# Kernel tuning notes

Hardware: AMD Instinct MI355X
Metric: run time of the kernel (lower is better)

## Reference

```python
import jax, jax.numpy as jnp
import numpy as np

D_MODEL = 1024
HEADS = 16
D_K = D_MODEL // HEADS


def setup_inputs() -> dict:
    key = jax.random.key(0)
    ks = jax.random.split(key, 11)
    bs, seq = 2, 2048
    scale = 1.0 / np.sqrt(D_MODEL)
    inp = {
        "query": jax.random.normal(ks[0], (bs, seq, D_MODEL), jnp.float32),
        "key": jax.random.normal(ks[1], (bs, seq, D_MODEL), jnp.float32),
        "value": jax.random.normal(ks[2], (bs, seq, D_MODEL), jnp.float32),
        # nn.Linear weights: y = x @ W.T + b, W shape [out, in]
        "Wq": jax.random.normal(ks[3], (D_MODEL, D_MODEL), jnp.float32) * scale,
        "bq": jnp.zeros((D_MODEL,), jnp.float32),
        "Wk": jax.random.normal(ks[4], (D_MODEL, D_MODEL), jnp.float32) * scale,
        "bk": jnp.zeros((D_MODEL,), jnp.float32),
        "Wv": jax.random.normal(ks[5], (D_MODEL, D_MODEL), jnp.float32) * scale,
        "bv": jnp.zeros((D_MODEL,), jnp.float32),
        "Wo": jax.random.normal(ks[6], (D_MODEL, D_MODEL), jnp.float32) * scale,
        "bo": jnp.zeros((D_MODEL,), jnp.float32),
    }
    return inp


def _split_heads(x, bs):
    # [b, s, d_model] -> [b, h, s, d_k]
    return x.reshape(bs, -1, HEADS, D_K).transpose(0, 2, 1, 3)


def reference(query, key, value, Wq, bq, Wk, bk, Wv, bv, Wo, bo):
    bs = query.shape[0]
    q = _split_heads(query @ Wq.T + bq, bs)
    k = _split_heads(key @ Wk.T + bk, bs)
    v = _split_heads(value @ Wv.T + bv, bs)
    # scaled dot-product attention (dropout is identity at eval)
    logits = jnp.einsum("bhqd,bhkd->bhqk", q, k) / np.sqrt(D_K).astype(np.float32)
    probs = jax.nn.softmax(logits, axis=-1)
    scores = jnp.einsum("bhqk,bhkd->bhqd", probs, v)  # [b, h, s, d_k]
    concat = scores.transpose(0, 2, 1, 3).reshape(bs, -1, D_MODEL)
    output = concat @ Wo.T + bo
    return (output, scores)
```

## Files before the change

kernel.cpp:

```cpp
#include <hip/hip_runtime.h>
#include <stdint.h>
#include <math.h>

typedef __bf16 bf16;
typedef __bf16 bf16x4 __attribute__((ext_vector_type(4)));
typedef __bf16 bf16x8 __attribute__((ext_vector_type(8)));
typedef float floatx4 __attribute__((ext_vector_type(4)));

#define CEXP 0.1803368801111204f

__global__ __launch_bounds__(256) void wcvt_kernel(
    const float* __restrict__ Wq, const float* __restrict__ Wk,
    const float* __restrict__ Wv, const float* __restrict__ Wo,
    bf16* __restrict__ dst)
{
  const float* src = (blockIdx.y == 0) ? Wq : (blockIdx.y == 1) ? Wk
                   : (blockIdx.y == 2) ? Wv : Wo;
  bf16* d = dst + (size_t)blockIdx.y * 1048576;
  const int i = (blockIdx.x * 256 + threadIdx.x) * 4;
  const floatx4 v = *(const floatx4*)(src + i);
  bf16x4 o;
#pragma unroll
  for (int j = 0; j < 4; ++j) o[j] = (bf16)v[j];
  *(bf16x4*)(d + i) = o;
}

__device__ __forceinline__ void gemm_body(
    const float* __restrict__ A, const bf16* __restrict__ Ab,
    const bf16* __restrict__ Wb, const float* __restrict__ bias,
    void* __restrict__ Cout, const int mode, const float oscale)
{
  __shared__ __align__(16) bf16 As[128 * 72];
  __shared__ __align__(16) bf16 Bs[128 * 72];
  const int tid  = threadIdx.x;
  const int wave = tid >> 6;
  const int lane = tid & 63;
  const int mlane = lane & 15;
  const int quad  = lane >> 4;
  const int m0 = blockIdx.x * 128;
  const int n0 = blockIdx.y * 128;
  const int wm = (wave >> 1) * 64;
  const int wn = (wave & 1) * 64;
  const int arow = tid >> 4, ac4 = (tid & 15) * 4;
  const int wrow = tid >> 3, wc8 = (tid & 7) * 8;

  floatx4 a_pf[8];
  bf16x8  ab_pf[4];
  bf16x8  w_pf[4];

  auto load_a = [&](int k0) {
    if (mode == 1) {
#pragma unroll
      for (int c = 0; c < 4; ++c) {
        const int token = m0 + c * 32 + wrow;
        const int b = token >> 11, s = token & 2047;
        const int h = k0 >> 6;
        ab_pf[c] = *(const bf16x8*)(Ab + (((size_t)(b * 16 + h) * 2048 + s) << 6) + wc8);
      }
    } else {
#pragma unroll
      for (int rr = 0; rr < 8; ++rr)
        a_pf[rr] = *(const floatx4*)(A + (size_t)(m0 + rr * 16 + arow) * 1024 + k0 + ac4);
    }
  };
  auto load_w = [&](int k0) {
#pragma unroll
    for (int c = 0; c < 4; ++c)
      w_pf[c] = *(const bf16x8*)(Wb + (size_t)(n0 + c * 32 + wrow) * 1024 + k0 + wc8);
  };

  load_a(0);
  load_w(0);

  floatx4 acc[4][4] = {};

  for (int k0 = 0; k0 < 1024; k0 += 64) {
    if (mode == 1) {
#pragma unroll
      for (int c = 0; c < 4; ++c)
        *(bf16x8*)&As[(c * 32 + wrow) * 72 + wc8] = ab_pf[c];
    } else {
#pragma unroll
      for (int rr = 0; rr < 8; ++rr) {
        bf16x4 ac;
#pragma unroll
        for (int j = 0; j < 4; ++j) ac[j] = (bf16)a_pf[rr][j];
        *(bf16x4*)&As[(rr * 16 + arow) * 72 + ac4] = ac;
      }
    }
#pragma unroll
    for (int c = 0; c < 4; ++c)
      *(bf16x8*)&Bs[(c * 32 + wrow) * 72 + wc8] = w_pf[c];
    __syncthreads();

    if (k0 + 64 < 1024) { load_a(k0 + 64); load_w(k0 + 64); }

#pragma unroll
    for (int kk = 0; kk < 64; kk += 32) {
      bf16x8 af[4], bfr[4];
#pragma unroll
      for (int t = 0; t < 4; ++t) {
        af[t]  = *(const bf16x8*)&As[(wm + t * 16 + mlane) * 72 + kk + quad * 8];
        bfr[t] = *(const bf16x8*)&Bs[(wn + t * 16 + mlane) * 72 + kk + quad * 8];
      }
#pragma unroll
      for (int mt = 0; mt < 4; ++mt)
#pragma unroll
        for (int nt = 0; nt < 4; ++nt)
          acc[mt][nt] = __builtin_amdgcn_mfma_f32_16x16x32_bf16(
              af[mt], bfr[nt], acc[mt][nt], 0, 0, 0);
    }
    __syncthreads();
  }

  if (mode == 2) {
    bf16* T = (wave < 2) ? &As[wave * 4608] : &Bs[(wave - 2) * 4608];
#pragma unroll
    for (int nt = 0; nt < 4; ++nt) {
      const float bv = bias[n0 + wn + nt * 16 + mlane];
#pragma unroll
      for (int mt = 0; mt < 4; ++mt) {
        bf16x4 t4;
#pragma unroll
        for (int r = 0; r < 4; ++r)
          t4[r] = (bf16)((acc[mt][nt][r] + bv) * oscale);
        *(bf16x4*)&T[(nt * 16 + mlane) * 72 + mt * 16 + quad * 4] = t4;
      }
    }
    asm volatile("s_waitcnt lgkmcnt(0)" ::: "memory");
    const int token0 = m0 + wm;
    const int bb = token0 >> 11;
    const int srow0 = token0 & 2047;
    const int h = (n0 + wn) >> 6;
    const int dl = lane >> 3;
    const int s8 = (lane & 7) * 8;
    bf16* outp = (bf16*)Cout + ((size_t)(bb * 16 + h) << 17);
#pragma unroll
    for (int p = 0; p < 8; ++p) {
      const int dk = p * 8 + dl;
      const bf16x8 v8 = *(const bf16x8*)&T[dk * 72 + s8];
      *(bf16x8*)&outp[((size_t)dk << 11) + srow0 + s8] = v8;
    }
    return;
  }

#pragma unroll
  for (int nt = 0; nt < 4; ++nt) {
    const int col = n0 + wn + nt * 16 + mlane;
    const float bv = bias[col];
#pragma unroll
    for (int mt = 0; mt < 4; ++mt) {
#pragma unroll
      for (int r = 0; r < 4; ++r) {
        const int row = m0 + wm + mt * 16 + quad * 4 + r;
        const float v = (acc[mt][nt][r] + bv) * oscale;
        if (mode == 0) {
          const int b = row >> 11, s = row & 2047;
          const int h = col >> 6, dk = col & 63;
          ((bf16*)Cout)[(((size_t)(b * 16 + h) * 2048 + s) << 6) + dk] = (bf16)v;
        } else {
          ((float*)Cout)[(size_t)row * 1024 + col] = v;
        }
      }
    }
  }
}

__global__ __launch_bounds__(256) void qkv_kernel(
    const float* __restrict__ q, const float* __restrict__ k, const float* __restrict__ v,
    const bf16* __restrict__ Wb,
    const float* __restrict__ bq, const float* __restrict__ bk, const float* __restrict__ bv,
    bf16* __restrict__ Qw, bf16* __restrict__ Kw, bf16* __restrict__ Vw)
{
  const int z = blockIdx.z;
  const float* A = (z == 0) ? q : (z == 1) ? k : v;
  const bf16* W  = Wb + (size_t)z * 1048576;
  const float* B = (z == 0) ? bq : (z == 1) ? bk : bv;
  if (z == 2)      gemm_body(A, nullptr, W, B, Vw, 2, 1.0f);
  else if (z == 1) gemm_body(A, nullptr, W, B, Kw, 0, 1.0f);
  else             gemm_body(A, nullptr, W, B, Qw, 0, CEXP);
}

__global__ __launch_bounds__(256) void out_kernel(
    const bf16* __restrict__ Sb, const bf16* __restrict__ Wob,
    const float* __restrict__ bo, float* __restrict__ out)
{
  gemm_body(nullptr, Sb, Wob, bo, out, 1, 1.0f);
}

__global__ __launch_bounds__(256) void attn_kernel(
    const bf16* __restrict__ Qw, const bf16* __restrict__ Kw,
    const bf16* __restrict__ Vtg, float* __restrict__ scores,
    bf16* __restrict__ Sb)
{
  __shared__ __align__(16) bf16 Ks[64 * 72];
  __shared__ __align__(16) bf16 Vt[64 * 72];
  __shared__ __align__(16) bf16 Ps[4][16 * 72];

  const int tid  = threadIdx.x;
  const int wave = tid >> 6;
  const int lane = tid & 63;
  const int mlane = lane & 15;
  const int quad  = lane >> 4;

  const int g = blockIdx.x + (blockIdx.y << 5);
  const int slot = g >> 3;
  const int bh = ((g & 7) << 2) + (slot >> 5);
  const int q0 = (slot & 31) << 6;
  const size_t base = (size_t)bh << 17;

  const int srow = tid >> 3, sc8 = (tid & 7) * 8;

  bf16x8 qf[2];
#pragma unroll
  for (int c = 0; c < 2; ++c)
    qf[c] = *(const bf16x8*)
        &Qw[base + (size_t)(q0 + wave * 16 + mlane) * 64 + c * 32 + quad * 8];

  bf16x8 ones;
#pragma unroll
  for (int j = 0; j < 8; ++j) ones[j] = (bf16)1.0f;

  floatx4 o[4] = {};
  floatx4 osum = {};

  bf16x8 kpf[2], vpf[2];
  auto load_kv = [&](int kt) {
#pragma unroll
    for (int rr = 0; rr < 2; ++rr) {
      const int row = rr * 32 + srow;
      kpf[rr] = *(const bf16x8*)&Kw[base + (size_t)(kt + row) * 64 + sc8];
      vpf[rr] = *(const bf16x8*)&Vtg[base + (size_t)row * 2048 + kt + sc8];
    }
  };
  load_kv(0);

  for (int kt = 0; kt < 2048; kt += 64) {
    __syncthreads();
#pragma unroll
    for (int rr = 0; rr < 2; ++rr) {
      const int row = rr * 32 + srow;
      *(bf16x8*)&Ks[row * 72 + sc8] = kpf[rr];
      *(bf16x8*)&Vt[row * 72 + sc8] = vpf[rr];
    }
    __syncthreads();
    if (kt + 64 < 2048) load_kv(kt + 64);

#pragma unroll
    for (int nt = 0; nt < 4; ++nt) {
      bf16x8 a0 = *(const bf16x8*)&Ks[(nt * 16 + mlane) * 72 + quad * 8];
      bf16x8 a1 = *(const bf16x8*)&Ks[(nt * 16 + mlane) * 72 + 32 + quad * 8];
      floatx4 s0 = {};
      __builtin_amdgcn_s_setprio(1);
      s0 = __builtin_amdgcn_mfma_f32_16x16x32_bf16(a0, qf[0], s0, 0, 0, 0);
      s0 = __builtin_amdgcn_mfma_f32_16x16x32_bf16(a1, qf[1], s0, 0, 0, 0);
      __builtin_amdgcn_s_setprio(0);
      bf16x4 pk;
#pragma unroll
      for (int r = 0; r < 4; ++r) pk[r] = (bf16)exp2f(s0[r]);
      *(bf16x4*)&Ps[wave][mlane * 72 + nt * 16 + quad * 4] = pk;
    }

    asm volatile("s_waitcnt lgkmcnt(0)" ::: "memory");

    bf16x8 pa0 = *(const bf16x8*)&Ps[wave][mlane * 72 + quad * 8];
    bf16x8 pa1 = *(const bf16x8*)&Ps[wave][mlane * 72 + 32 + quad * 8];
    __builtin_amdgcn_s_setprio(1);
    osum = __builtin_amdgcn_mfma_f32_16x16x32_bf16(pa0, ones, osum, 0, 0, 0);
    osum = __builtin_amdgcn_mfma_f32_16x16x32_bf16(pa1, ones, osum, 0, 0, 0);
#pragma unroll
    for (int nt = 0; nt < 4; ++nt) {
      bf16x8 vb0 = *(const bf16x8*)&Vt[(nt * 16 + mlane) * 72 + quad * 8];
      bf16x8 vb1 = *(const bf16x8*)&Vt[(nt * 16 + mlane) * 72 + 32 + quad * 8];
      o[nt] = __builtin_amdgcn_mfma_f32_16x16x32_bf16(pa0, vb0, o[nt], 0, 0, 0);
      o[nt] = __builtin_amdgcn_mfma_f32_16x16x32_bf16(pa1, vb1, o[nt], 0, 0, 0);
    }
    __builtin_amdgcn_s_setprio(0);
  }

#pragma unroll
  for (int r = 0; r < 4; ++r) {
    const float inv = 1.0f / osum[r];
    const int row = q0 + wave * 16 + quad * 4 + r;
#pragma unroll
    for (int nt = 0; nt < 4; ++nt) {
      const float val = o[nt][r] * inv;
      const size_t idx = base + (size_t)row * 64 + nt * 16 + mlane;
      scores[idx] = val;
      Sb[idx] = (bf16)val;
    }
  }
}

extern "C" void kernel_launch(void* const* d_in, const int* in_sizes, int n_in,
                              void* d_out, int out_size, void* d_ws, size_t ws_size,
                              hipStream_t stream) {
  const float* query = (const float*)d_in[0];
  const float* key   = (const float*)d_in[1];
  const float* value = (const float*)d_in[2];
  const float* Wq = (const float*)d_in[3];
  const float* bq = (const float*)d_in[4];
  const float* Wk = (const float*)d_in[5];
  const float* bk = (const float*)d_in[6];
  const float* Wv = (const float*)d_in[7];
  const float* bv = (const float*)d_in[8];
  const float* Wo = (const float*)d_in[9];
  const float* bo = (const float*)d_in[10];

  float* out    = (float*)d_out;
  float* scores = out + (size_t)4194304;

  bf16* Wb  = (bf16*)d_ws;
  bf16* Qws = Wb + (size_t)4194304;
  bf16* Kws = Qws + (size_t)4194304;
  bf16* Vws = Kws + (size_t)4194304;
  bf16* Sb  = Vws + (size_t)4194304;

  wcvt_kernel<<<dim3(1024, 4), 256, 0, stream>>>(Wq, Wk, Wv, Wo, Wb);
  qkv_kernel<<<dim3(32, 8, 3), 256, 0, stream>>>(query, key, value, Wb,
                                                 bq, bk, bv, Qws, Kws, Vws);
  attn_kernel<<<dim3(32, 32), 256, 0, stream>>>(Qws, Kws, Vws, scores, Sb);
  out_kernel<<<dim3(32, 8), 256, 0, stream>>>(Sb, Wb + (size_t)3145728, bo, out);
}
```

Before: 242.9 us.

## Restructure attention kernel with 32x32 MFMA, 128-query tiles and split-K wave reduction

Each attention block now handles 128 queries instead of 64. The four waves split the work as two query halves by two key halves, and the partial outputs and row sums are reduced through shared memory at the end. The kernel moves from 16x16x32 to 32x32x16 bf16 MFMAs, computes row sums in scalar code instead of with a ones-matrix MFMA, and swaps the padded LDS layout for XOR-swizzled rows. This doubles reuse of each loaded K/V tile and cuts per-tile MFMA overhead. The cost is more registers (launch bounds set to 2), a larger LDS footprint for the reduction buffers, and half as many blocks.

```diff
diff --git a/kernel.cpp b/kernel.cpp
--- a/kernel.cpp
+++ b/kernel.cpp
@@ -6,6 +6,7 @@
 typedef __bf16 bf16x4 __attribute__((ext_vector_type(4)));
 typedef __bf16 bf16x8 __attribute__((ext_vector_type(8)));
 typedef float floatx4 __attribute__((ext_vector_type(4)));
+typedef float floatx16 __attribute__((ext_vector_type(16)));
 
 #define CEXP 0.1803368801111204f
 
@@ -188,49 +189,53 @@
   gemm_body(nullptr, Sb, Wob, bo, out, 1, 1.0f);
 }
 
-__global__ __launch_bounds__(256) void attn_kernel(
+__global__ __launch_bounds__(256, 2) void attn_kernel(
     const bf16* __restrict__ Qw, const bf16* __restrict__ Kw,
     const bf16* __restrict__ Vtg, float* __restrict__ scores,
     bf16* __restrict__ Sb)
 {
-  __shared__ __align__(16) bf16 Ks[64 * 72];
-  __shared__ __align__(16) bf16 Vt[64 * 72];
-  __shared__ __align__(16) bf16 Ps[4][16 * 72];
+  __shared__ __align__(16) char smem[32768];
+  __shared__ __align__(16) float Ored[2][64][64];
+  __shared__ float RSred[2][64][2];
 
   const int tid  = threadIdx.x;
   const int wave = tid >> 6;
   const int lane = tid & 63;
-  const int mlane = lane & 15;
-  const int quad  = lane >> 4;
-
-  const int g = blockIdx.x + (blockIdx.y << 5);
+  const int c    = lane & 31;
+  const int hi   = lane >> 5;
+
+  const int g = blockIdx.x + (blockIdx.y << 4);
   const int slot = g >> 3;
-  const int bh = ((g & 7) << 2) + (slot >> 5);
-  const int q0 = (slot & 31) << 6;
+  const int bh = ((g & 7) << 2) + (slot >> 4);
+  const int q0 = (slot & 15) << 7;
   const size_t base = (size_t)bh << 17;
 
-  const int srow = tid >> 3, sc8 = (tid & 7) * 8;
-
-  bf16x8 qf[2];
-#pragma unroll
-  for (int c = 0; c < 2; ++c)
-    qf[c] = *(const bf16x8*)
-        &Qw[base + (size_t)(q0 + wave * 16 + mlane) * 64 + c * 32 + quad * 8];
-
-  bf16x8 ones;
-#pragma unroll
-  for (int j = 0; j < 8; ++j) ones[j] = (bf16)1.0f;
-
-  floatx4 o[4] = {};
-  floatx4 osum = {};
+  const int qh = (wave & 1) * 64;
+  const int kh = (wave >> 1) * 32;
+
+  const int srow = tid >> 3;
+  const int scb  = (tid & 7) * 16;
+
+  char* Pw = smem + 16384 + wave * 4096;
+
+  bf16x8 qf[2][4];
+#pragma unroll
+  for (int qt = 0; qt < 2; ++qt)
+#pragma unroll
+    for (int m = 0; m < 4; ++m)
+      qf[qt][m] = *(const bf16x8*)
+          &Qw[base + (size_t)(q0 + qh + qt * 32 + c) * 64 + m * 16 + hi * 8];
+
+  floatx16 o[2][2] = {};
+  float rs[2] = {0.f, 0.f};
 
   bf16x8 kpf[2], vpf[2];
   auto load_kv = [&](int kt) {
 #pragma unroll
     for (int rr = 0; rr < 2; ++rr) {
       const int row = rr * 32 + srow;
-      kpf[rr] = *(const bf16x8*)&Kw[base + (size_t)(kt + row) * 64 + sc8];
-      vpf[rr] = *(const bf16x8*)&Vtg[base + (size_t)row * 2048 + kt + sc8];
+      kpf[rr] = *(const bf16x8*)&Kw[base + (size_t)(kt + row) * 64 + (tid & 7) * 8];
+      vpf[rr] = *(const bf16x8*)&Vtg[base + (size_t)row * 2048 + kt + (tid & 7) * 8];
     }
   };
   load_kv(0);
@@ -240,55 +245,122 @@
 #pragma unroll
     for (int rr = 0; rr < 2; ++rr) {
       const int row = rr * 32 + srow;
-      *(bf16x8*)&Ks[row * 72 + sc8] = kpf[rr];
-      *(bf16x8*)&Vt[row * 72 + sc8] = vpf[rr];
+      const int swz = (row & 7) << 4;
+      *(bf16x8*)(smem +        row * 128 + (scb ^ swz)) = kpf[rr];
+      *(bf16x8*)(smem + 8192 + row * 128 + (scb ^ swz)) = vpf[rr];
     }
     __syncthreads();
     if (kt + 64 < 2048) load_kv(kt + 64);
 
-#pragma unroll
-    for (int nt = 0; nt < 4; ++nt) {
-      bf16x8 a0 = *(const bf16x8*)&Ks[(nt * 16 + mlane) * 72 + quad * 8];
-      bf16x8 a1 = *(const bf16x8*)&Ks[(nt * 16 + mlane) * 72 + 32 + quad * 8];
-      floatx4 s0 = {};
+    floatx16 s[2] = {};
+    {
+      const int row = kh + c;
+      const int swz = (row & 7) << 4;
       __builtin_amdgcn_s_setprio(1);
-      s0 = __builtin_amdgcn_mfma_f32_16x16x32_bf16(a0, qf[0], s0, 0, 0, 0);
-      s0 = __builtin_amdgcn_mfma_f32_16x16x32_bf16(a1, qf[1], s0, 0, 0, 0);
+#pragma unroll
+      for (int m = 0; m < 4; ++m) {
+        const bf16x8 a = *(const bf16x8*)(smem + row * 128 + ((m * 32 + hi * 16) ^ swz));
+        s[0] = __builtin_amdgcn_mfma_f32_32x32x16_bf16(a, qf[0][m], s[0], 0, 0, 0);
+        s[1] = __builtin_amdgcn_mfma_f32_32x32x16_bf16(a, qf[1][m], s[1], 0, 0, 0);
+      }
       __builtin_amdgcn_s_setprio(0);
-      bf16x4 pk;
-#pragma unroll
-      for (int r = 0; r < 4; ++r) pk[r] = (bf16)exp2f(s0[r]);
-      *(bf16x4*)&Ps[wave][mlane * 72 + nt * 16 + quad * 4] = pk;
-    }
-
-    asm volatile("s_waitcnt lgkmcnt(0)" ::: "memory");
-
-    bf16x8 pa0 = *(const bf16x8*)&Ps[wave][mlane * 72 + quad * 8];
-    bf16x8 pa1 = *(const bf16x8*)&Ps[wave][mlane * 72 + 32 + quad * 8];
+    }
+
+#pragma unroll
+    for (int qt = 0; qt < 2; ++qt) {
+      char* pr = Pw + (qt * 32 + c) * 64;
+      const int psw = (c & 3) << 4;
+#pragma unroll
+      for (int gg = 0; gg < 4; ++gg) {
+        bf16x4 pk;
+#pragma unroll
+        for (int i = 0; i < 4; ++i) {
+          const float p = exp2f(s[qt][gg * 4 + i]);
+          rs[qt] += p;
+          pk[i] = (bf16)p;
+        }
+        *(bf16x4*)(pr + ((gg * 16 + hi * 8) ^ psw)) = pk;
+      }
+    }
+
     __builtin_amdgcn_s_setprio(1);
-    osum = __builtin_amdgcn_mfma_f32_16x16x32_bf16(pa0, ones, osum, 0, 0, 0);
-    osum = __builtin_amdgcn_mfma_f32_16x16x32_bf16(pa1, ones, osum, 0, 0, 0);
-#pragma unroll
-    for (int nt = 0; nt < 4; ++nt) {
-      bf16x8 vb0 = *(const bf16x8*)&Vt[(nt * 16 + mlane) * 72 + quad * 8];
-      bf16x8 vb1 = *(const bf16x8*)&Vt[(nt * 16 + mlane) * 72 + 32 + quad * 8];
-      o[nt] = __builtin_amdgcn_mfma_f32_16x16x32_bf16(pa0, vb0, o[nt], 0, 0, 0);
-      o[nt] = __builtin_amdgcn_mfma_f32_16x16x32_bf16(pa1, vb1, o[nt], 0, 0, 0);
+#pragma unroll
+    for (int t = 0; t < 2; ++t) {
+      bf16x8 pb[2];
+#pragma unroll
+      for (int qt = 0; qt < 2; ++qt)
+        pb[qt] = *(const bf16x8*)(Pw + (qt * 32 + c) * 64 + ((t * 32 + hi * 16) ^ ((c & 3) << 4)));
+#pragma unroll
+      for (int d = 0; d < 2; ++d) {
+        const int row = d * 32 + c;
+        const bf16x8 va = *(const bf16x8*)
+            (smem + 8192 + row * 128 + ((kh * 2 + t * 32 + hi * 16) ^ ((row & 7) << 4)));
+        o[d][0] = __builtin_amdgcn_mfma_f32_32x32x16_bf16(va, pb[0], o[d][0], 0, 0, 0);
+        o[d][1] = __builtin_amdgcn_mfma_f32_32x32x16_bf16(va, pb[1], o[d][1], 0, 0, 0);
+      }
     }
     __builtin_amdgcn_s_setprio(0);
   }
 
-#pragma unroll
-  for (int r = 0; r < 4; ++r) {
-    const float inv = 1.0f / osum[r];
-    const int row = q0 + wave * 16 + quad * 4 + r;
-#pragma unroll
-    for (int nt = 0; nt < 4; ++nt) {
-      const float val = o[nt][r] * inv;
-      const size_t idx = base + (size_t)row * 64 + nt * 16 + mlane;
-      scores[idx] = val;
-      Sb[idx] = (bf16)val;
-    }
+  rs[0] += __shfl_xor(rs[0], 32, 64);
+  rs[1] += __shfl_xor(rs[1], 32, 64);
+
+  if (wave >= 2) {
+#pragma unroll
+    for (int d = 0; d < 2; ++d)
+#pragma unroll
+      for (int qt = 0; qt < 2; ++qt)
+#pragma unroll
+        for (int gg = 0; gg < 4; ++gg) {
+          floatx4 w4;
+#pragma unroll
+          for (int i = 0; i < 4; ++i) w4[i] = o[d][qt][gg * 4 + i];
+          *(floatx4*)&Ored[wave - 2][lane][(d * 2 + qt) * 16 + gg * 4] = w4;
+        }
+    RSred[wave - 2][lane][0] = rs[0];
+    RSred[wave - 2][lane][1] = rs[1];
+  }
+  __syncthreads();
+  if (wave >= 2) return;
+
+#pragma unroll
+  for (int d = 0; d < 2; ++d)
+#pragma unroll
+    for (int qt = 0; qt < 2; ++qt)
+#pragma unroll
+      for (int gg = 0; gg < 4; ++gg) {
+        const floatx4 r4 = *(const floatx4*)&Ored[wave][lane][(d * 2 + qt) * 16 + gg * 4];
+#pragma unroll
+        for (int i = 0; i < 4; ++i) o[d][qt][gg * 4 + i] += r4[i];
+      }
+  rs[0] += RSred[wave][lane][0];
+  rs[1] += RSred[wave][lane][1];
+
+  const float inv0 = 1.0f / rs[0];
+  const float inv1 = 1.0f / rs[1];
+
+#pragma unroll
+  for (int qt = 0; qt < 2; ++qt) {
+    const float inv = qt ? inv1 : inv0;
+    const int q = q0 + qh + qt * 32 + c;
+    float* sr = scores + base + (size_t)q * 64;
+    bf16*  br = Sb + base + (size_t)q * 64;
+#pragma unroll
+    for (int d = 0; d < 2; ++d)
+#pragma unroll
+      for (int gg = 0; gg < 4; ++gg) {
+        const int dk = d * 32 + gg * 8 + hi * 4;
+        floatx4 v4;
+        bf16x4 b4;
+#pragma unroll
+        for (int i = 0; i < 4; ++i) {
+          const float v = o[d][qt][gg * 4 + i] * inv;
+          v4[i] = v;
+          b4[i] = (bf16)v;
+        }
+        *(floatx4*)(sr + dk) = v4;
+        *(bf16x4*)(br + dk) = b4;
+      }
   }
 }
 
@@ -319,6 +391,6 @@
   wcvt_kernel<<<dim3(1024, 4), 256, 0, stream>>>(Wq, Wk, Wv, Wo, Wb);
   qkv_kernel<<<dim3(32, 8, 3), 256, 0, stream>>>(query, key, value, Wb,
                                                  bq, bk, bv, Qws, Kws, Vws);
-  attn_kernel<<<dim3(32, 32), 256, 0, stream>>>(Qws, Kws, Vws, scores, Sb);
+  attn_kernel<<<dim3(16, 32), 256, 0, stream>>>(Qws, Kws, Vws, scores, Sb);
   out_kernel<<<dim3(32, 8), 256, 0, stream>>>(Sb, Wb + (size_t)3145728, bo, out);
 }
```

After: 245.2 us. About the same (+1.0%).

## Rewrite attention with 32x32 MFMA and register-resident probabilities via permlane swap

Applied to the files above, without the earlier changes.

The attention kernel now uses 32x32x16 bf16 MFMA tiles with 128 queries per block (32 per wave), halving the grid. Softmax probabilities stay in registers: they are packed with v_cvt_pk_bf16_f32 and rearranged with v_permlane32_swap instead of round-tripping through a shared-memory P buffer. The row sum is accumulated in scalar registers instead of an extra MFMA against ones. This cuts LDS traffic and MFMA count per tile, at the cost of higher register pressure and fewer blocks in the grid.

```diff
diff --git a/kernel.cpp b/kernel.cpp
--- a/kernel.cpp
+++ b/kernel.cpp
@@ -6,6 +6,7 @@
 typedef __bf16 bf16x4 __attribute__((ext_vector_type(4)));
 typedef __bf16 bf16x8 __attribute__((ext_vector_type(8)));
 typedef float floatx4 __attribute__((ext_vector_type(4)));
+typedef float floatx16 __attribute__((ext_vector_type(16)));
 
 #define CEXP 0.1803368801111204f
 
@@ -188,108 +189,140 @@
   gemm_body(nullptr, Sb, Wob, bo, out, 1, 1.0f);
 }
 
-__global__ __launch_bounds__(256) void attn_kernel(
+__global__ __launch_bounds__(256, 2) void attn_kernel(
     const bf16* __restrict__ Qw, const bf16* __restrict__ Kw,
     const bf16* __restrict__ Vtg, float* __restrict__ scores,
     bf16* __restrict__ Sb)
 {
-  __shared__ __align__(16) bf16 Ks[64 * 72];
-  __shared__ __align__(16) bf16 Vt[64 * 72];
-  __shared__ __align__(16) bf16 Ps[4][16 * 72];
+  __shared__ __align__(16) char smem[2 * 64 * 136];
+  char* KsB = smem;
+  char* VsB = smem + 64 * 136;
 
   const int tid  = threadIdx.x;
   const int wave = tid >> 6;
   const int lane = tid & 63;
-  const int mlane = lane & 15;
-  const int quad  = lane >> 4;
-
-  const int g = blockIdx.x + (blockIdx.y << 5);
+  const int c    = lane & 31;
+  const int hi   = lane >> 5;
+
+  const int g = blockIdx.x + (blockIdx.y << 4);
   const int slot = g >> 3;
-  const int bh = ((g & 7) << 2) + (slot >> 5);
-  const int q0 = (slot & 31) << 6;
+  const int bh = ((g & 7) << 2) + (slot >> 4);
+  const int q0 = (slot & 15) << 7;
   const size_t base = (size_t)bh << 17;
 
-  const int srow = tid >> 3, sc8 = (tid & 7) * 8;
-
-  bf16x8 qf[2];
-#pragma unroll
-  for (int c = 0; c < 2; ++c)
-    qf[c] = *(const bf16x8*)
-        &Qw[base + (size_t)(q0 + wave * 16 + mlane) * 64 + c * 32 + quad * 8];
-
-  bf16x8 ones;
-#pragma unroll
-  for (int j = 0; j < 8; ++j) ones[j] = (bf16)1.0f;
-
-  floatx4 o[4] = {};
-  floatx4 osum = {};
+  const int srow = tid >> 2;
+  const int sce  = (tid & 3) * 16;
+
+  bf16x8 qf[4];
+#pragma unroll
+  for (int m = 0; m < 4; ++m)
+    qf[m] = *(const bf16x8*)
+        &Qw[base + (size_t)(q0 + wave * 32 + c) * 64 + m * 16 + hi * 8];
+
+  floatx16 o[2] = {};
+  float rs = 0.f;
 
   bf16x8 kpf[2], vpf[2];
   auto load_kv = [&](int kt) {
-#pragma unroll
-    for (int rr = 0; rr < 2; ++rr) {
-      const int row = rr * 32 + srow;
-      kpf[rr] = *(const bf16x8*)&Kw[base + (size_t)(kt + row) * 64 + sc8];
-      vpf[rr] = *(const bf16x8*)&Vtg[base + (size_t)row * 2048 + kt + sc8];
-    }
+    const bf16* kp = &Kw[base + (size_t)(kt + srow) * 64 + sce];
+    kpf[0] = *(const bf16x8*)kp;
+    kpf[1] = *(const bf16x8*)(kp + 8);
+    const bf16* vp = &Vtg[base + (size_t)srow * 2048 + kt + sce];
+    vpf[0] = *(const bf16x8*)vp;
+    vpf[1] = *(const bf16x8*)(vp + 8);
   };
   load_kv(0);
 
   for (int kt = 0; kt < 2048; kt += 64) {
     __syncthreads();
-#pragma unroll
-    for (int rr = 0; rr < 2; ++rr) {
-      const int row = rr * 32 + srow;
-      *(bf16x8*)&Ks[row * 72 + sc8] = kpf[rr];
-      *(bf16x8*)&Vt[row * 72 + sc8] = vpf[rr];
+    {
+      char* kr = KsB + srow * 136 + (tid & 3) * 32;
+      char* vr = VsB + srow * 136 + (tid & 3) * 32;
+      *(bf16x4*)(kr +  0) = ((const bf16x4*)&kpf[0])[0];
+      *(bf16x4*)(kr +  8) = ((const bf16x4*)&kpf[0])[1];
+      *(bf16x4*)(kr + 16) = ((const bf16x4*)&kpf[1])[0];
+      *(bf16x4*)(kr + 24) = ((const bf16x4*)&kpf[1])[1];
+      *(bf16x4*)(vr +  0) = ((const bf16x4*)&vpf[0])[0];
+      *(bf16x4*)(vr +  8) = ((const bf16x4*)&vpf[0])[1];
+      *(bf16x4*)(vr + 16) = ((const bf16x4*)&vpf[1])[0];
+      *(bf16x4*)(vr + 24) = ((const bf16x4*)&vpf[1])[1];
     }
     __syncthreads();
     if (kt + 64 < 2048) load_kv(kt + 64);
 
 #pragma unroll
-    for (int nt = 0; nt < 4; ++nt) {
-      bf16x8 a0 = *(const bf16x8*)&Ks[(nt * 16 + mlane) * 72 + quad * 8];
-      bf16x8 a1 = *(const bf16x8*)&Ks[(nt * 16 + mlane) * 72 + 32 + quad * 8];
-      floatx4 s0 = {};
+    for (int ks = 0; ks < 2; ++ks) {
+      const char* krow = KsB + (ks * 32 + c) * 136;
+      floatx16 s = {};
       __builtin_amdgcn_s_setprio(1);
-      s0 = __builtin_amdgcn_mfma_f32_16x16x32_bf16(a0, qf[0], s0, 0, 0, 0);
-      s0 = __builtin_amdgcn_mfma_f32_16x16x32_bf16(a1, qf[1], s0, 0, 0, 0);
+#pragma unroll
+      for (int m = 0; m < 4; ++m) {
+        bf16x8 a;
+        ((bf16x4*)&a)[0] = *(const bf16x4*)(krow + m * 32 + hi * 16);
+        ((bf16x4*)&a)[1] = *(const bf16x4*)(krow + m * 32 + hi * 16 + 8);
+        s = __builtin_amdgcn_mfma_f32_32x32x16_bf16(a, qf[m], s, 0, 0, 0);
+      }
       __builtin_amdgcn_s_setprio(0);
-      bf16x4 pk;
-#pragma unroll
-      for (int r = 0; r < 4; ++r) pk[r] = (bf16)exp2f(s0[r]);
-      *(bf16x4*)&Ps[wave][mlane * 72 + nt * 16 + quad * 4] = pk;
-    }
-
-    asm volatile("s_waitcnt lgkmcnt(0)" ::: "memory");
-
-    bf16x8 pa0 = *(const bf16x8*)&Ps[wave][mlane * 72 + quad * 8];
-    bf16x8 pa1 = *(const bf16x8*)&Ps[wave][mlane * 72 + 32 + quad * 8];
-    __builtin_amdgcn_s_setprio(1);
-    osum = __builtin_amdgcn_mfma_f32_16x16x32_bf16(pa0, ones, osum, 0, 0, 0);
-    osum = __builtin_amdgcn_mfma_f32_16x16x32_bf16(pa1, ones, osum, 0, 0, 0);
-#pragma unroll
-    for (int nt = 0; nt < 4; ++nt) {
-      bf16x8 vb0 = *(const bf16x8*)&Vt[(nt * 16 + mlane) * 72 + quad * 8];
-      bf16x8 vb1 = *(const bf16x8*)&Vt[(nt * 16 + mlane) * 72 + 32 + quad * 8];
-      o[nt] = __builtin_amdgcn_mfma_f32_16x16x32_bf16(pa0, vb0, o[nt], 0, 0, 0);
-      o[nt] = __builtin_amdgcn_mfma_f32_16x16x32_bf16(pa1, vb1, o[nt], 0, 0, 0);
-    }
-    __builtin_amdgcn_s_setprio(0);
+
+      float p[16];
+#pragma unroll
+      for (int i = 0; i < 16; ++i) p[i] = exp2f(s[i]);
+#pragma unroll
+      for (int i = 0; i < 16; ++i) rs += p[i];
+
+      uint32_t ulo[4], uhi[4];
+#pragma unroll
+      for (int gg = 0; gg < 4; ++gg) {
+        asm("v_cvt_pk_bf16_f32 %0, %1, %2"
+            : "=v"(ulo[gg]) : "v"(p[4 * gg]), "v"(p[4 * gg + 1]));
+        asm("v_cvt_pk_bf16_f32 %0, %1, %2"
+            : "=v"(uhi[gg]) : "v"(p[4 * gg + 2]), "v"(p[4 * gg + 3]));
+      }
+
+      __builtin_amdgcn_s_setprio(1);
+#pragma unroll
+      for (int t = 0; t < 2; ++t) {
+        uint32_t w0 = ulo[2 * t], w2 = ulo[2 * t + 1];
+        uint32_t w1 = uhi[2 * t], w3 = uhi[2 * t + 1];
+        asm("v_permlane32_swap_b32 %0, %1" : "+v"(w0), "+v"(w2));
+        asm("v_permlane32_swap_b32 %0, %1" : "+v"(w1), "+v"(w3));
+        union { bf16x8 v; uint32_t w[4]; } pu;
+        pu.w[0] = w0; pu.w[1] = w1; pu.w[2] = w2; pu.w[3] = w3;
+#pragma unroll
+        for (int d = 0; d < 2; ++d) {
+          const char* vrow = VsB + (d * 32 + c) * 136 + ks * 64 + t * 32 + hi * 16;
+          bf16x8 va;
+          ((bf16x4*)&va)[0] = *(const bf16x4*)(vrow);
+          ((bf16x4*)&va)[1] = *(const bf16x4*)(vrow + 8);
+          o[d] = __builtin_amdgcn_mfma_f32_32x32x16_bf16(va, pu.v, o[d], 0, 0, 0);
+        }
+      }
+      __builtin_amdgcn_s_setprio(0);
+    }
   }
 
-#pragma unroll
-  for (int r = 0; r < 4; ++r) {
-    const float inv = 1.0f / osum[r];
-    const int row = q0 + wave * 16 + quad * 4 + r;
-#pragma unroll
-    for (int nt = 0; nt < 4; ++nt) {
-      const float val = o[nt][r] * inv;
-      const size_t idx = base + (size_t)row * 64 + nt * 16 + mlane;
-      scores[idx] = val;
-      Sb[idx] = (bf16)val;
-    }
-  }
+  rs += __shfl_xor(rs, 32, 64);
+  const float inv = 1.0f / rs;
+
+  const int q = q0 + wave * 32 + c;
+  float* sr = scores + base + (size_t)q * 64;
+  bf16*  br = Sb + base + (size_t)q * 64;
+#pragma unroll
+  for (int d = 0; d < 2; ++d)
+#pragma unroll
+    for (int gg = 0; gg < 4; ++gg) {
+      const int dk = d * 32 + gg * 8 + hi * 4;
+      floatx4 v4;
+      bf16x4 b4;
+#pragma unroll
+      for (int i = 0; i < 4; ++i) {
+        const float v = o[d][gg * 4 + i] * inv;
+        v4[i] = v;
+        b4[i] = (bf16)v;
+      }
+      *(floatx4*)(sr + dk) = v4;
+      *(bf16x4*)(br + dk) = b4;
+    }
 }
 
 extern "C" void kernel_launch(void* const* d_in, const int* in_sizes, int n_in,
@@ -319,6 +352,6 @@
   wcvt_kernel<<<dim3(1024, 4), 256, 0, stream>>>(Wq, Wk, Wv, Wo, Wb);
   qkv_kernel<<<dim3(32, 8, 3), 256, 0, stream>>>(query, key, value, Wb,
                                                  bq, bk, bv, Qws, Kws, Vws);
-  attn_kernel<<<dim3(32, 32), 256, 0, stream>>>(Qws, Kws, Vws, scores, Sb);
+  attn_kernel<<<dim3(16, 32), 256, 0, stream>>>(Qws, Kws, Vws, scores, Sb);
   out_kernel<<<dim3(32, 8), 256, 0, stream>>>(Sb, Wb + (size_t)3145728, bo, out);
 }
```

Result: faster. 237.5 us (-2.2%).
